# Kernel optimization log

Measured on AMD Instinct MI355X. Metric: run time of the kernel, lower is better.

The kernel has to match this reference:

```python
import jax, jax.numpy as jnp
import numpy as np

B, S, R, H = 64, 256, 196, 1024

def setup_inputs() -> dict:
    key = jax.random.key(0)
    ks = jax.random.split(key, 12)
    s = 0.02
    return {
        "dns_feature": jax.random.normal(ks[0], (B, S, H), jnp.float32),
        "img_features": jax.random.normal(ks[1], (B, R, H), jnp.float32),
        "W_dns1": jax.random.normal(ks[2], (H, H), jnp.float32) * s,
        "b_dns1": jax.random.normal(ks[3], (H,), jnp.float32) * s,
        "W_img1": jax.random.normal(ks[4], (H, H), jnp.float32) * s,
        "w_att1": jax.random.normal(ks[5], (2 * H,), jnp.float32) * s,
        "b_att1": jax.random.normal(ks[6], (), jnp.float32) * s,
        "W_dns2": jax.random.normal(ks[7], (H, H), jnp.float32) * s,
        "W_img2": jax.random.normal(ks[8], (H, H), jnp.float32) * s,
        "b_img2": jax.random.normal(ks[9], (H,), jnp.float32) * s,
        "w_att2": jax.random.normal(ks[10], (2 * H,), jnp.float32) * s,
        "b_att2": jax.random.normal(ks[11], (), jnp.float32) * s,
    }

def reference(dns_feature, img_features, W_dns1, b_dns1, W_img1, w_att1, b_att1,
              W_dns2, W_img2, b_img2, w_att2, b_att2):
    h = W_dns1.shape[0]
    # --- stage 1: textual attention (img queries over dns positions) ---
    # tanh(concat([img_proj, dns_proj])) then 2H->1 linear decomposes into
    # per-side dot products + broadcast add (repeat is position-wise redundant).
    dns_p1 = jnp.tanh(jnp.einsum('bsh,oh->bso', dns_feature, W_dns1) + b_dns1)  # (B,S,H)
    img_p1 = jnp.tanh(jnp.einsum('brh,oh->bro', img_features, W_img1))          # (B,R,H)
    s_img = img_p1 @ w_att1[:h]   # (B,R)  concat order: [img, dns]
    s_dns = dns_p1 @ w_att1[h:]   # (B,S)
    scores1 = s_img[:, :, None] + s_dns[:, None, :] + b_att1                    # (B,R,S)
    a1 = jax.nn.softmax(scores1, axis=-1)
    att_dns = jnp.einsum('brs,bsh->brh', a1, dns_feature)                       # (B,R,H)
    # --- stage 2: visual attention (attended-dns queries over img regions) ---
    dns_p2 = jnp.tanh(jnp.einsum('brh,oh->bro', att_dns, W_dns2))               # (B,R,H)
    img_p2 = jnp.tanh(jnp.einsum('brh,oh->bro', img_features, W_img2) + b_img2) # (B,R,H)
    t_dns = dns_p2 @ w_att2[:h]   # (B,R)  concat order: [dns, img]
    t_img = img_p2 @ w_att2[h:]   # (B,R)
    scores2 = t_dns[:, :, None] + t_img[:, None, :] + b_att2                    # (B,R,R)
    a2 = jax.nn.softmax(scores2, axis=-1)
    att_img = jnp.einsum('bij,bjh->bih', a2, img_features)                      # (B,R,H)
    return att_img, att_dns
```

## Files before the change

### kernel.cpp

```cpp
#include <hip/hip_runtime.h>

#define Hdim 1024
#define BB 64
#define SS 256
#define RR 196
#define MD (BB * SS)
#define MI (BB * RR)

typedef __attribute__((ext_vector_type(8))) short short8;
typedef __attribute__((ext_vector_type(4))) float floatx4;
typedef unsigned short us;

__device__ __forceinline__ unsigned short f2bf(float f) {
  unsigned int u = __float_as_uint(f);
  unsigned int r = 0x7FFFu + ((u >> 16) & 1u);
  return (unsigned short)((u + r) >> 16);
}

__device__ __forceinline__ float fast_tanh(float x) {
  x = fminf(15.f, fmaxf(-15.f, x));
  float e = __expf(2.f * x);
  return (e - 1.f) / (e + 1.f);
}

#define GLOAD16(g, l) __builtin_amdgcn_global_load_lds( \
    (const __attribute__((address_space(1))) unsigned int*)(g), \
    (__attribute__((address_space(3))) unsigned int*)(l), 16, 0, 0)

__global__ __launch_bounds__(256) void f32_to_bf16_kn(
    const float4* __restrict__ in, uint4* __restrict__ out, int n16)
{
  int i = blockIdx.x * 256 + threadIdx.x;
  const int stride = gridDim.x * 256;
  for (; i < n16; i += stride) {
    const float4 a = in[2 * i];
    const float4 b = in[2 * i + 1];
    uint4 o;
    o.x = (unsigned)f2bf(a.x) | ((unsigned)f2bf(a.y) << 16);
    o.y = (unsigned)f2bf(a.z) | ((unsigned)f2bf(a.w) << 16);
    o.z = (unsigned)f2bf(b.x) | ((unsigned)f2bf(b.y) << 16);
    o.w = (unsigned)f2bf(b.z) | ((unsigned)f2bf(b.w) << 16);
    out[i] = o;
  }
}

__global__ __launch_bounds__(256) void gemm_score_bf(
    const us* __restrict__ Xb, const us* __restrict__ Wb,
    const float* __restrict__ bias, const float* __restrict__ vatt,
    float* __restrict__ scores)
{
  __shared__ us Ash[128 * 64];
  __shared__ us Bsh[128 * 64];

  const int q  = gridDim.x >> 3;
  const int wg = (blockIdx.x & 7) * q + (blockIdx.x >> 3);
  const long m0 = (long)(wg >> 3) * 128;
  const long n0 = (long)(wg & 7) * 128;

  const int tid  = threadIdx.x;
  const int lane = tid & 63;
  const int wave = tid >> 6;
  const int waveM = (wave >> 1) * 64;
  const int waveN = (wave & 1) * 64;

  const int rowSub  = lane >> 3;
  const int srcColE = (((lane & 7) ^ rowSub)) * 8;

  const us* gA[4]; const us* gB[4];
  const us* lA[4]; const us* lB[4];
  #pragma unroll
  for (int c = 0; c < 4; ++c) {
    const int r = (wave * 4 + c) * 8 + rowSub;
    gA[c] = Xb + (m0 + r) * Hdim + srcColE;
    gB[c] = Wb + (n0 + r) * Hdim + srcColE;
    lA[c] = Ash + (wave * 4 + c) * 512 + lane * 8;
    lB[c] = Bsh + (wave * 4 + c) * 512 + lane * 8;
  }

  floatx4 acc[4][4];
  #pragma unroll
  for (int i = 0; i < 4; ++i)
    #pragma unroll
    for (int j = 0; j < 4; ++j)
      acc[i][j] = (floatx4){0.f, 0.f, 0.f, 0.f};

  const int frow = lane & 15;
  const int g    = lane >> 4;
  const int sw   = frow & 7;

  for (int k0 = 0; k0 < Hdim; k0 += 64) {
    __syncthreads();
    #pragma unroll
    for (int c = 0; c < 4; ++c) {
      GLOAD16(gA[c] + k0, lA[c]);
      GLOAD16(gB[c] + k0, lB[c]);
    }
    __syncthreads();
    #pragma unroll
    for (int ks = 0; ks < 2; ++ks) {
      const int slot = ((ks * 4 + g) ^ sw) * 8;
      short8 afr[4], bfr[4];
      #pragma unroll
      for (int mf = 0; mf < 4; ++mf)
        afr[mf] = *(const short8*)(Ash + (waveM + mf * 16 + frow) * 64 + slot);
      #pragma unroll
      for (int nf = 0; nf < 4; ++nf)
        bfr[nf] = *(const short8*)(Bsh + (waveN + nf * 16 + frow) * 64 + slot);
      #pragma unroll
      for (int mf = 0; mf < 4; ++mf)
        #pragma unroll
        for (int nf = 0; nf < 4; ++nf)
          acc[mf][nf] = __builtin_amdgcn_mfma_f32_16x16x32_bf16(afr[mf], bfr[nf], acc[mf][nf], 0, 0, 0);
    }
  }

  const int rgrp = lane >> 4;
  #pragma unroll
  for (int mf = 0; mf < 4; ++mf) {
    float part[4] = {0.f, 0.f, 0.f, 0.f};
    #pragma unroll
    for (int nf = 0; nf < 4; ++nf) {
      const int n = (int)n0 + waveN + nf * 16 + (lane & 15);
      const float bi = bias[n];
      const float vv = vatt[n];
      #pragma unroll
      for (int j = 0; j < 4; ++j)
        part[j] += fast_tanh(acc[mf][nf][j] + bi) * vv;
    }
    #pragma unroll
    for (int j = 0; j < 4; ++j) {
      float s = part[j];
      s += __shfl_xor(s, 1);
      s += __shfl_xor(s, 2);
      s += __shfl_xor(s, 4);
      s += __shfl_xor(s, 8);
      if ((lane & 15) == 0) {
        const int m = (int)m0 + waveM + mf * 16 + rgrp * 4 + j;
        atomicAdd(&scores[m], s);
      }
    }
  }
}

__global__ __launch_bounds__(256) void gemm_score(
    const float* __restrict__ X, const float* __restrict__ W,
    const float* __restrict__ bias, const float* __restrict__ vatt,
    float* __restrict__ scores)
{
  __shared__ us Ash[128 * 32];
  __shared__ us Bsh[128 * 32];
  const int tid  = threadIdx.x;
  const int lane = tid & 63;
  const int wave = tid >> 6;
  const int waveM = (wave >> 1) * 64;
  const int waveN = (wave & 1) * 64;
  const long m0 = (long)blockIdx.x * 128;
  const long n0 = (long)blockIdx.y * 128;
  const int ldRow   = tid >> 3;
  const int ldChunk = (tid & 7) * 4;

  floatx4 acc[4][4];
  #pragma unroll
  for (int i = 0; i < 4; ++i)
    #pragma unroll
    for (int j = 0; j < 4; ++j)
      acc[i][j] = (floatx4){0.f, 0.f, 0.f, 0.f};

  const int frow = lane & 15;
  const int fk   = (lane >> 4) * 8;

  for (int k0 = 0; k0 < Hdim; k0 += 32) {
    __syncthreads();
    #pragma unroll
    for (int p = 0; p < 4; ++p) {
      const int r = ldRow + p * 32;
      const float4 av = *(const float4*)&X[(m0 + r) * Hdim + k0 + ldChunk];
      const float4 bv = *(const float4*)&W[(n0 + r) * Hdim + k0 + ldChunk];
      uint2 ap, bp;
      ap.x = (unsigned)f2bf(av.x) | ((unsigned)f2bf(av.y) << 16);
      ap.y = (unsigned)f2bf(av.z) | ((unsigned)f2bf(av.w) << 16);
      bp.x = (unsigned)f2bf(bv.x) | ((unsigned)f2bf(bv.y) << 16);
      bp.y = (unsigned)f2bf(bv.z) | ((unsigned)f2bf(bv.w) << 16);
      *(uint2*)&Ash[r * 32 + ldChunk] = ap;
      *(uint2*)&Bsh[r * 32 + ldChunk] = bp;
    }
    __syncthreads();
    short8 afr[4], bfr[4];
    #pragma unroll
    for (int mf = 0; mf < 4; ++mf)
      afr[mf] = *(const short8*)&Ash[(waveM + mf * 16 + frow) * 32 + fk];
    #pragma unroll
    for (int nf = 0; nf < 4; ++nf)
      bfr[nf] = *(const short8*)&Bsh[(waveN + nf * 16 + frow) * 32 + fk];
    #pragma unroll
    for (int mf = 0; mf < 4; ++mf)
      #pragma unroll
      for (int nf = 0; nf < 4; ++nf)
        acc[mf][nf] = __builtin_amdgcn_mfma_f32_16x16x32_bf16(afr[mf], bfr[nf], acc[mf][nf], 0, 0, 0);
  }

  const int rgrp = lane >> 4;
  #pragma unroll
  for (int mf = 0; mf < 4; ++mf) {
    float part[4] = {0.f, 0.f, 0.f, 0.f};
    #pragma unroll
    for (int nf = 0; nf < 4; ++nf) {
      const int n = (int)n0 + waveN + nf * 16 + (lane & 15);
      const float bi = bias[n];
      const float vv = vatt[n];
      #pragma unroll
      for (int j = 0; j < 4; ++j)
        part[j] += fast_tanh(acc[mf][nf][j] + bi) * vv;
    }
    #pragma unroll
    for (int j = 0; j < 4; ++j) {
      float s = part[j];
      s += __shfl_xor(s, 1);
      s += __shfl_xor(s, 2);
      s += __shfl_xor(s, 4);
      s += __shfl_xor(s, 8);
      if ((lane & 15) == 0) {
        const int m = (int)m0 + waveM + mf * 16 + rgrp * 4 + j;
        atomicAdd(&scores[m], s);
      }
    }
  }
}

template <int L>
__global__ __launch_bounds__(256) void softmax_attend_bcast(
    const float* __restrict__ scores, const float* __restrict__ feat,
    float* __restrict__ out)
{
  __shared__ float p[256];
  __shared__ float red[256];
  const int b  = blockIdx.x;
  const int h0 = blockIdx.y * 256;
  const int t  = threadIdx.x;

  const float sc = (t < L) ? scores[b * L + t] : -1e30f;
  red[t] = sc;
  __syncthreads();
  for (int off = 128; off > 0; off >>= 1) {
    if (t < off) red[t] = fmaxf(red[t], red[t + off]);
    __syncthreads();
  }
  const float mx = red[0];
  __syncthreads();
  const float e = (t < L) ? __expf(sc - mx) : 0.f;
  red[t] = e;
  __syncthreads();
  for (int off = 128; off > 0; off >>= 1) {
    if (t < off) red[t] += red[t + off];
    __syncthreads();
  }
  p[t] = e / red[0];
  __syncthreads();

  const int h = h0 + t;
  const float* fb = feat + (size_t)b * L * Hdim + h;
  float acc = 0.f;
  #pragma unroll 8
  for (int s = 0; s < L; ++s)
    acc += p[s] * fb[(size_t)s * Hdim];

  float* ob = out + (size_t)b * RR * Hdim + h;
  #pragma unroll 4
  for (int r = 0; r < RR; ++r)
    ob[(size_t)r * Hdim] = acc;
}

template <int L>
__global__ __launch_bounds__(256) void softmax_attend(
    const float* __restrict__ scores, const float* __restrict__ feat,
    float* __restrict__ attended)
{
  __shared__ float p[256];
  __shared__ float red[256];
  const int b  = blockIdx.x;
  const int h0 = blockIdx.y * 256;
  const int t  = threadIdx.x;

  const float sc = (t < L) ? scores[b * L + t] : -1e30f;
  red[t] = sc;
  __syncthreads();
  for (int off = 128; off > 0; off >>= 1) {
    if (t < off) red[t] = fmaxf(red[t], red[t + off]);
    __syncthreads();
  }
  const float mx = red[0];
  __syncthreads();
  const float e = (t < L) ? __expf(sc - mx) : 0.f;
  red[t] = e;
  __syncthreads();
  for (int off = 128; off > 0; off >>= 1) {
    if (t < off) red[t] += red[t + off];
    __syncthreads();
  }
  p[t] = e / red[0];
  __syncthreads();

  const int h = h0 + t;
  const float* fb = feat + (size_t)b * L * Hdim + h;
  float acc = 0.f;
  #pragma unroll 4
  for (int s = 0; s < L; ++s)
    acc += p[s] * fb[(size_t)s * Hdim];
  attended[b * Hdim + h] = acc;
}

__global__ __launch_bounds__(256) void broadcast_out(
    const float4* __restrict__ att_img, const float4* __restrict__ att_dns,
    float4* __restrict__ out)
{
  const int H4 = Hdim / 4;
  const long region_sz = (long)BB * RR * H4;
  const long total = 2 * region_sz;
  for (long i = (long)blockIdx.x * blockDim.x + threadIdx.x; i < total;
       i += (long)gridDim.x * blockDim.x) {
    const int region = (i >= region_sz);
    const long rem = i - (long)region * region_sz;
    const int b  = (int)(rem / (RR * H4));
    const int h4 = (int)(rem % H4);
    const float4* src = region ? att_dns : att_img;
    out[i] = src[b * H4 + h4];
  }
}

extern "C" void kernel_launch(void* const* d_in, const int* in_sizes, int n_in,
                              void* d_out, int out_size, void* d_ws, size_t ws_size,
                              hipStream_t stream) {
  const float* dns    = (const float*)d_in[0];
  const float* img    = (const float*)d_in[1];
  const float* W_dns1 = (const float*)d_in[2];
  const float* b_dns1 = (const float*)d_in[3];
  const float* w_att1 = (const float*)d_in[5];
  const float* W_img2 = (const float*)d_in[8];
  const float* b_img2 = (const float*)d_in[9];
  const float* w_att2 = (const float*)d_in[10];

  float* out_img = (float*)d_out;
  float* out_dns = (float*)d_out + (size_t)BB * RR * Hdim;

  const size_t dnsB = (size_t)MD * Hdim * 2;
  const size_t imgB = (size_t)MI * Hdim * 2;
  const size_t wB   = (size_t)Hdim * Hdim * 2;
  const size_t scoresB = (16384 + 12544) * sizeof(float);
  const size_t need = dnsB + imgB + 2 * wB + scoresB;

  dim3 blk(256);

  if (ws_size >= need) {
    char* cur = (char*)d_ws;
    us* dns_bf = (us*)cur; cur += dnsB;
    us* img_bf = (us*)cur; cur += imgB;
    us* Wd1_bf = (us*)cur; cur += wB;
    us* Wi2_bf = (us*)cur; cur += wB;
    float* s_dns = (float*)cur;
    float* t_img = s_dns + 16384;

    f32_to_bf16_kn<<<2048, blk, 0, stream>>>((const float4*)dns, (uint4*)dns_bf, MD * Hdim / 8);
    f32_to_bf16_kn<<<2048, blk, 0, stream>>>((const float4*)img, (uint4*)img_bf, MI * Hdim / 8);
    f32_to_bf16_kn<<<512,  blk, 0, stream>>>((const float4*)W_dns1, (uint4*)Wd1_bf, Hdim * Hdim / 8);
    f32_to_bf16_kn<<<512,  blk, 0, stream>>>((const float4*)W_img2, (uint4*)Wi2_bf, Hdim * Hdim / 8);

    hipMemsetAsync(s_dns, 0, scoresB, stream);

    gemm_score_bf<<<dim3((MD / 128) * 8), blk, 0, stream>>>(
        dns_bf, Wd1_bf, b_dns1, w_att1 + Hdim, s_dns);
    gemm_score_bf<<<dim3((MI / 128) * 8), blk, 0, stream>>>(
        img_bf, Wi2_bf, b_img2, w_att2 + Hdim, t_img);

    softmax_attend_bcast<SS><<<dim3(BB, Hdim / 256), blk, 0, stream>>>(s_dns, dns, out_dns);
    softmax_attend_bcast<RR><<<dim3(BB, Hdim / 256), blk, 0, stream>>>(t_img, img, out_img);
  } else {
    float* ws    = (float*)d_ws;
    float* s_dns = ws;
    float* t_img = ws + 16384;
    float* att_d = ws + 16384 + 12544;
    float* att_i = att_d + BB * Hdim;

    hipMemsetAsync(s_dns, 0, (16384 + 12544) * sizeof(float), stream);

    gemm_score<<<dim3(MD / 128, Hdim / 128), blk, 0, stream>>>(
        dns, W_dns1, b_dns1, w_att1 + Hdim, s_dns);
    gemm_score<<<dim3(MI / 128, Hdim / 128), blk, 0, stream>>>(
        img, W_img2, b_img2, w_att2 + Hdim, t_img);

    softmax_attend<SS><<<dim3(BB, Hdim / 256), blk, 0, stream>>>(s_dns, dns, att_d);
    softmax_attend<RR><<<dim3(BB, Hdim / 256), blk, 0, stream>>>(t_img, img, att_i);

    broadcast_out<<<2048, blk, 0, stream>>>((const float4*)att_i, (const float4*)att_d,
                                            (float4*)d_out);
  }
}
```

Baseline: 186.7 us.

## Fuse prep, GEMM and attend launches; read bf16 features in attention

New measurement: 167.2 us. -10.5%, faster.

```diff
diff --git a/kernel.cpp b/kernel.cpp
--- a/kernel.cpp
+++ b/kernel.cpp
@@ -27,35 +27,67 @@
     (const __attribute__((address_space(1))) unsigned int*)(g), \
     (__attribute__((address_space(3))) unsigned int*)(l), 16, 0, 0)
 
-__global__ __launch_bounds__(256) void f32_to_bf16_kn(
-    const float4* __restrict__ in, uint4* __restrict__ out, int n16)
-{
-  int i = blockIdx.x * 256 + threadIdx.x;
+__global__ __launch_bounds__(256) void prep_kernel(
+    const float4* __restrict__ dns, const float4* __restrict__ img,
+    const float4* __restrict__ Wd1, const float4* __restrict__ Wi2,
+    uint4* __restrict__ dns_bf, uint4* __restrict__ img_bf,
+    uint4* __restrict__ wd1_bf, uint4* __restrict__ wi2_bf,
+    float4* __restrict__ scz)
+{
+  constexpr int N0 = (MD * Hdim) / 8;
+  constexpr int N1 = N0 + (MI * Hdim) / 8;
+  constexpr int N2 = N1 + (Hdim * Hdim) / 8;
+  constexpr int N3 = N2 + (Hdim * Hdim) / 8;
+  constexpr int N4 = N3 + (MD + MI) / 8;
   const int stride = gridDim.x * 256;
-  for (; i < n16; i += stride) {
-    const float4 a = in[2 * i];
-    const float4 b = in[2 * i + 1];
-    uint4 o;
-    o.x = (unsigned)f2bf(a.x) | ((unsigned)f2bf(a.y) << 16);
-    o.y = (unsigned)f2bf(a.z) | ((unsigned)f2bf(a.w) << 16);
-    o.z = (unsigned)f2bf(b.x) | ((unsigned)f2bf(b.y) << 16);
-    o.w = (unsigned)f2bf(b.z) | ((unsigned)f2bf(b.w) << 16);
-    out[i] = o;
-  }
-}
-
-__global__ __launch_bounds__(256) void gemm_score_bf(
-    const us* __restrict__ Xb, const us* __restrict__ Wb,
-    const float* __restrict__ bias, const float* __restrict__ vatt,
-    float* __restrict__ scores)
+  for (int i = blockIdx.x * 256 + threadIdx.x; i < N4; i += stride) {
+    if (i < N3) {
+      const float4* src; uint4* dst; int li;
+      if (i < N0)      { src = dns; dst = dns_bf; li = i; }
+      else if (i < N1) { src = img; dst = img_bf; li = i - N0; }
+      else if (i < N2) { src = Wd1; dst = wd1_bf; li = i - N1; }
+      else             { src = Wi2; dst = wi2_bf; li = i - N2; }
+      const float4 a = src[2 * li];
+      const float4 b = src[2 * li + 1];
+      uint4 o;
+      o.x = (unsigned)f2bf(a.x) | ((unsigned)f2bf(a.y) << 16);
+      o.y = (unsigned)f2bf(a.z) | ((unsigned)f2bf(a.w) << 16);
+      o.z = (unsigned)f2bf(b.x) | ((unsigned)f2bf(b.y) << 16);
+      o.w = (unsigned)f2bf(b.z) | ((unsigned)f2bf(b.w) << 16);
+      dst[li] = o;
+    } else {
+      const int li = i - N3;
+      const float4 z4 = {0.f, 0.f, 0.f, 0.f};
+      scz[2 * li]     = z4;
+      scz[2 * li + 1] = z4;
+    }
+  }
+}
+
+__global__ __launch_bounds__(256) void gemm_score_bf2(
+    const us* __restrict__ X1, const us* __restrict__ W1,
+    const float* __restrict__ bias1, const float* __restrict__ v1, float* sc1,
+    const us* __restrict__ X2, const us* __restrict__ W2,
+    const float* __restrict__ bias2, const float* __restrict__ v2, float* sc2)
 {
   __shared__ us Ash[128 * 64];
   __shared__ us Bsh[128 * 64];
 
   const int q  = gridDim.x >> 3;
   const int wg = (blockIdx.x & 7) * q + (blockIdx.x >> 3);
-  const long m0 = (long)(wg >> 3) * 128;
-  const long n0 = (long)(wg & 7) * 128;
+
+  const us* Xb; const us* Wb; const float* bias; const float* vatt; float* scores;
+  int mt, nt;
+  if (wg < (MD / 128) * 8) {
+    Xb = X1; Wb = W1; bias = bias1; vatt = v1; scores = sc1;
+    mt = wg >> 3; nt = wg & 7;
+  } else {
+    const int w2 = wg - (MD / 128) * 8;
+    Xb = X2; Wb = W2; bias = bias2; vatt = v2; scores = sc2;
+    mt = w2 >> 3; nt = w2 & 7;
+  }
+  const long m0 = (long)mt * 128;
+  const long n0 = (long)nt * 128;
 
   const int tid  = threadIdx.x;
   const int lane = tid & 63;
@@ -140,6 +172,60 @@
       }
     }
   }
+}
+
+__global__ __launch_bounds__(256) void attend_bcast(
+    const float* __restrict__ sc_d, const us* __restrict__ dns_bf,
+    const float* __restrict__ sc_i, const us* __restrict__ img_bf,
+    float* __restrict__ out)
+{
+  __shared__ float p[256];
+  __shared__ float red[256];
+  const int b  = blockIdx.x;
+  const int h0 = blockIdx.y * 512;
+  const int z  = blockIdx.z;
+  const int L  = z ? RR : SS;
+  const float* scores = z ? sc_i : sc_d;
+  const us*    feat   = z ? img_bf : dns_bf;
+  float* outp = out + (z ? (size_t)0 : (size_t)BB * RR * Hdim);
+  const int t = threadIdx.x;
+
+  const float sc = (t < L) ? scores[b * L + t] : -1e30f;
+  red[t] = sc;
+  __syncthreads();
+  for (int off = 128; off > 0; off >>= 1) {
+    if (t < off) red[t] = fmaxf(red[t], red[t + off]);
+    __syncthreads();
+  }
+  const float mx = red[0];
+  __syncthreads();
+  const float e = (t < L) ? __expf(sc - mx) : 0.f;
+  red[t] = e;
+  __syncthreads();
+  for (int off = 128; off > 0; off >>= 1) {
+    if (t < off) red[t] += red[t + off];
+    __syncthreads();
+  }
+  p[t] = e / red[0];
+  __syncthreads();
+
+  const int h = h0 + 2 * t;
+  const us* fb = feat + (size_t)b * L * Hdim + h;
+  float a0 = 0.f, a1 = 0.f;
+  #pragma unroll 8
+  for (int s = 0; s < L; ++s) {
+    const unsigned u = *(const unsigned*)(fb + (size_t)s * Hdim);
+    const float f0 = __uint_as_float(u << 16);
+    const float f1 = __uint_as_float(u & 0xffff0000u);
+    a0 += p[s] * f0;
+    a1 += p[s] * f1;
+  }
+
+  float* ob = outp + (size_t)b * RR * Hdim + h;
+  const float2 v = make_float2(a0, a1);
+  #pragma unroll 4
+  for (int r = 0; r < RR; ++r)
+    *(float2*)(ob + (size_t)r * Hdim) = v;
 }
 
 __global__ __launch_bounds__(256) void gemm_score(
@@ -228,49 +314,6 @@
 }
 
 template <int L>
-__global__ __launch_bounds__(256) void softmax_attend_bcast(
-    const float* __restrict__ scores, const float* __restrict__ feat,
-    float* __restrict__ out)
-{
-  __shared__ float p[256];
-  __shared__ float red[256];
-  const int b  = blockIdx.x;
-  const int h0 = blockIdx.y * 256;
-  const int t  = threadIdx.x;
-
-  const float sc = (t < L) ? scores[b * L + t] : -1e30f;
-  red[t] = sc;
-  __syncthreads();
-  for (int off = 128; off > 0; off >>= 1) {
-    if (t < off) red[t] = fmaxf(red[t], red[t + off]);
-    __syncthreads();
-  }
-  const float mx = red[0];
-  __syncthreads();
-  const float e = (t < L) ? __expf(sc - mx) : 0.f;
-  red[t] = e;
-  __syncthreads();
-  for (int off = 128; off > 0; off >>= 1) {
-    if (t < off) red[t] += red[t + off];
-    __syncthreads();
-  }
-  p[t] = e / red[0];
-  __syncthreads();
-
-  const int h = h0 + t;
-  const float* fb = feat + (size_t)b * L * Hdim + h;
-  float acc = 0.f;
-  #pragma unroll 8
-  for (int s = 0; s < L; ++s)
-    acc += p[s] * fb[(size_t)s * Hdim];
-
-  float* ob = out + (size_t)b * RR * Hdim + h;
-  #pragma unroll 4
-  for (int r = 0; r < RR; ++r)
-    ob[(size_t)r * Hdim] = acc;
-}
-
-template <int L>
 __global__ __launch_bounds__(256) void softmax_attend(
     const float* __restrict__ scores, const float* __restrict__ feat,
     float* __restrict__ attended)
@@ -339,9 +382,6 @@
   const float* b_img2 = (const float*)d_in[9];
   const float* w_att2 = (const float*)d_in[10];
 
-  float* out_img = (float*)d_out;
-  float* out_dns = (float*)d_out + (size_t)BB * RR * Hdim;
-
   const size_t dnsB = (size_t)MD * Hdim * 2;
   const size_t imgB = (size_t)MI * Hdim * 2;
   const size_t wB   = (size_t)Hdim * Hdim * 2;
@@ -359,20 +399,18 @@
     float* s_dns = (float*)cur;
     float* t_img = s_dns + 16384;
 
-    f32_to_bf16_kn<<<2048, blk, 0, stream>>>((const float4*)dns, (uint4*)dns_bf, MD * Hdim / 8);
-    f32_to_bf16_kn<<<2048, blk, 0, stream>>>((const float4*)img, (uint4*)img_bf, MI * Hdim / 8);
-    f32_to_bf16_kn<<<512,  blk, 0, stream>>>((const float4*)W_dns1, (uint4*)Wd1_bf, Hdim * Hdim / 8);
-    f32_to_bf16_kn<<<512,  blk, 0, stream>>>((const float4*)W_img2, (uint4*)Wi2_bf, Hdim * Hdim / 8);
-
-    hipMemsetAsync(s_dns, 0, scoresB, stream);
-
-    gemm_score_bf<<<dim3((MD / 128) * 8), blk, 0, stream>>>(
-        dns_bf, Wd1_bf, b_dns1, w_att1 + Hdim, s_dns);
-    gemm_score_bf<<<dim3((MI / 128) * 8), blk, 0, stream>>>(
+    prep_kernel<<<2048, blk, 0, stream>>>(
+        (const float4*)dns, (const float4*)img,
+        (const float4*)W_dns1, (const float4*)W_img2,
+        (uint4*)dns_bf, (uint4*)img_bf, (uint4*)Wd1_bf, (uint4*)Wi2_bf,
+        (float4*)s_dns);
+
+    gemm_score_bf2<<<dim3((MD / 128 + MI / 128) * 8), blk, 0, stream>>>(
+        dns_bf, Wd1_bf, b_dns1, w_att1 + Hdim, s_dns,
         img_bf, Wi2_bf, b_img2, w_att2 + Hdim, t_img);
 
-    softmax_attend_bcast<SS><<<dim3(BB, Hdim / 256), blk, 0, stream>>>(s_dns, dns, out_dns);
-    softmax_attend_bcast<RR><<<dim3(BB, Hdim / 256), blk, 0, stream>>>(t_img, img, out_img);
+    attend_bcast<<<dim3(BB, Hdim / 512, 2), blk, 0, stream>>>(
+        s_dns, dns_bf, t_img, img_bf, (float*)d_out);
   } else {
     float* ws    = (float*)d_ws;
     float* s_dns = ws;
```
